# Kernel tuning notes

Hardware: AMD Instinct MI355X
Metric: run time of the kernel (lower is better)

## Reference

```python
import jax, jax.numpy as jnp
import numpy as np

D_MODEL = 1024
NUM_HEADS = 16
D_K = D_MODEL // NUM_HEADS
THETA = 10000.0
B, S = 2, 2048


def setup_inputs() -> dict:
    key = jax.random.key(0)
    k_x, k_q, k_k, k_v, k_o = jax.random.split(key, 5)
    std = np.sqrt(2.0 / (D_MODEL + D_MODEL))
    x = jax.random.normal(k_x, (B, S, D_MODEL), dtype=jnp.float32)
    # positions: per-row arange 0..S-1 (must stay < max_seq_len)
    token_positions = jnp.broadcast_to(jnp.arange(S, dtype=jnp.int32), (B, S))
    mk = lambda k: (jax.random.normal(k, (D_MODEL, D_MODEL), dtype=jnp.float32) * std)
    return {
        'x': x,
        'token_positions': token_positions,
        'Wq': mk(k_q), 'Wk': mk(k_k), 'Wv': mk(k_v), 'Wo': mk(k_o),
    }


def _rope(x, pos):
    # x: [B, H, S, D_K], pos: [B, S] int
    inv_freq = 1.0 / (THETA ** (jnp.arange(0, D_K, 2, dtype=jnp.float32) / D_K))  # [D_K/2]
    angles = pos.astype(jnp.float32)[..., None] * inv_freq  # [B, S, D_K/2]
    cos = jnp.cos(angles)[:, None, :, :]  # [B, 1, S, D_K/2]
    sin = jnp.sin(angles)[:, None, :, :]
    x_even = x[..., 0::2]
    x_odd = x[..., 1::2]
    out_even = x_even * cos - x_odd * sin
    out_odd = x_even * sin + x_odd * cos
    # interleave back: [..., D_K/2, 2] -> [..., D_K]
    return jnp.stack([out_even, out_odd], axis=-1).reshape(x.shape)


def reference(x, token_positions, Wq, Wk, Wv, Wo):
    b, s, d = x.shape
    h, dk = NUM_HEADS, D_K
    # projections: weight is [d_out, d_in], y = x W^T
    q = jnp.einsum('bsd,ed->bse', x, Wq).reshape(b, s, h, dk).transpose(0, 2, 1, 3)
    k = jnp.einsum('bsd,ed->bse', x, Wk).reshape(b, s, h, dk).transpose(0, 2, 1, 3)
    v = jnp.einsum('bsd,ed->bse', x, Wv).reshape(b, s, h, dk).transpose(0, 2, 1, 3)
    q = _rope(q, token_positions)
    k = _rope(k, token_positions)
    scores = jnp.einsum('bhqd,bhkd->bhqk', q, k) / jnp.sqrt(jnp.float32(dk))
    causal = jnp.tril(jnp.ones((s, s), dtype=bool))
    scores = jnp.where(causal, scores, -jnp.inf)
    weights = jax.nn.softmax(scores, axis=-1)
    attn = jnp.einsum('bhqk,bhkd->bhqd', weights, v)  # [B,H,S,D_K]
    concat = attn.transpose(0, 2, 1, 3).reshape(b, s, d)
    return jnp.einsum('bsd,ed->bse', concat, Wo)
```

## Files before the change

### kernel.cpp

```cpp
#include <hip/hip_runtime.h>
#include <hip/hip_bf16.h>

#define BB 2
#define SS 2048
#define DD 1024
#define HH 16
#define DKK 64
#define MM (BB * SS)
#define PER ((size_t)MM * DD)

typedef __bf16 v8bf __attribute__((ext_vector_type(8)));
typedef float  v4f  __attribute__((ext_vector_type(4)));

__device__ __forceinline__ float bf2f(unsigned int u16) {
    union { unsigned int i; float f; } x;
    x.i = u16 << 16;
    return x.f;
}
__device__ __forceinline__ unsigned int pack2(float a, float b) {
    union { __hip_bfloat16 h; unsigned short u; } x, y;
    x.h = __float2bfloat16(a); y.h = __float2bfloat16(b);
    return (unsigned int)x.u | ((unsigned int)y.u << 16);
}
__device__ __forceinline__ unsigned short f2bfu(float v) {
    union { __hip_bfloat16 h; unsigned short u; } x;
    x.h = __float2bfloat16(v);
    return x.u;
}
template<bool BF>
__device__ __forceinline__ void ld4(const void* p, size_t i, float* f) {
    if (BF) {
        const uint2 u = *(const uint2*)((const unsigned short*)p + i);
        f[0] = bf2f(u.x & 0xffffu); f[1] = bf2f(u.x >> 16);
        f[2] = bf2f(u.y & 0xffffu); f[3] = bf2f(u.y >> 16);
    } else {
        const float4 v = *(const float4*)((const float*)p + i);
        f[0] = v.x; f[1] = v.y; f[2] = v.z; f[3] = v.w;
    }
}
template<bool BF>
__device__ __forceinline__ void st1(void* p, size_t i, float v) {
    if (BF) ((__hip_bfloat16*)p)[i] = __float2bfloat16(v);
    else    ((float*)p)[i] = v;
}
template<bool BF>
__device__ __forceinline__ uint4 ld8bf(const void* p, size_t i) {
    if (BF) return *(const uint4*)((const unsigned short*)p + i);
    float f[8];
    ld4<false>(p, i, f);
    ld4<false>(p, i + 4, f + 4);
    uint4 u;
    u.x = pack2(f[0], f[1]); u.y = pack2(f[2], f[3]);
    u.z = pack2(f[4], f[5]); u.w = pack2(f[6], f[7]);
    return u;
}

typedef const __attribute__((address_space(1))) void* gas_p;
typedef __attribute__((address_space(3))) void* las_p;
__device__ __forceinline__ void gld16(const void* g, void* l) {
    __builtin_amdgcn_global_load_lds(
        (gas_p)(unsigned long long)g,
        (las_p)(unsigned int)(unsigned long long)l,
        16, 0, 0);
}

__device__ __forceinline__ bool sniff_bf(const void* x) {
    const unsigned int w = ((const unsigned int*)x)[threadIdx.x & 63];
    const int e = (w >> 7) & 0xFF;
    return __popcll(__ballot(e >= 100 && e <= 140)) >= 32;
}

__global__ __launch_bounds__(256) void precast(
    const void* __restrict__ X,  const void* __restrict__ Wq,
    const void* __restrict__ Wk, const void* __restrict__ Wv,
    const void* __restrict__ Wo, unsigned short* __restrict__ out,
    float* __restrict__ tab)
{
    const int bid = blockIdx.x;
    const int tid = threadIdx.x;

    if (bid >= 4096) {
        const int idx = (bid - 4096) * 256 + tid;
        const int s = idx >> 5;
        const int f = idx & 31;
        const float invf = __expf((float)f * -0.2878231366f);
        const float ang = (float)s * invf;
        float sn, cs;
        __sincosf(ang, &sn, &cs);
        ((float2*)tab)[idx] = make_float2(cs, sn);
        return;
    }

    const void* src;
    size_t off;
    unsigned short* dst;
    if (bid < 2048) {
        src = X;
        off = (size_t)bid * 2048;
        dst = out + off;
    } else {
        const int w  = (bid - 2048) >> 9;
        const size_t lo = (size_t)((bid - 2048) & 511) * 2048;
        src = (w == 0) ? Wq : (w == 1) ? Wk : (w == 2) ? Wv : Wo;
        off = lo;
        dst = out + PER + (size_t)w * (DD * DD) + lo;
    }
    const bool bf = sniff_bf(src);
    const size_t i = off + (size_t)tid * 8;
    if (bf) {
        *(uint4*)(dst + tid * 8) = *(const uint4*)((const unsigned short*)src + i);
    } else {
        float f[8];
        ld4<false>(src, i, f);
        ld4<false>(src, i + 4, f + 4);
        uint4 u;
        u.x = pack2(f[0], f[1]); u.y = pack2(f[2], f[3]);
        u.z = pack2(f[4], f[5]); u.w = pack2(f[6], f[7]);
        *(uint4*)(dst + tid * 8) = u;
    }
}

template<bool BF, bool TAB>
__device__ __forceinline__ void qkv_body128(
    const void* __restrict__ X,
    const void* __restrict__ Wq, const void* __restrict__ Wk, const void* __restrict__ Wv,
    const int* __restrict__ pos, const float* __restrict__ tab,
    __hip_bfloat16* __restrict__ Qb, __hip_bfloat16* __restrict__ Kb,
    __hip_bfloat16* __restrict__ Vb,
    unsigned short* Sh)
{
    const int tid  = threadIdx.x;
    const int lane = tid & 63;
    const int wv   = tid >> 6;
    const int wr   = wv >> 1;
    const int wc   = wv & 1;
    const int ln   = lane & 15;
    const int qd   = lane >> 4;
    const int srow = lane >> 2;
    const int sc4  = lane & 3;

    const int m0  = blockIdx.x * 128;
    const int n0g = blockIdx.y * 128;
    const int z   = n0g >> 10;
    const int nw  = n0g & (DD - 1);
    const void* W = (z == 0) ? Wq : (z == 1) ? Wk : Wv;

    unsigned short* A0 = Sh;
    unsigned short* A1 = Sh + 4096;
    unsigned short* B0 = Sh + 8192;
    unsigned short* B1 = Sh + 12288;

    auto stage = [&](int k0, unsigned short* Ad, unsigned short* Bd) {
#pragma unroll
        for (int g = 0; g < 2; ++g) {
            const int base = (wv * 2 + g) * 16;
            const int row  = base + srow;
            const int sc   = sc4 ^ ((row >> 1) & 3);
            const size_t ga = (size_t)(m0 + row) * DD + k0 + sc * 8;
            if (BF) gld16((const unsigned short*)X + ga, Ad + (size_t)base * 32);
            else    *(uint4*)(Ad + (size_t)row * 32 + sc4 * 8) = ld8bf<false>(X, ga);
            const size_t gb = (size_t)(nw + row) * DD + k0 + sc * 8;
            if (BF) gld16((const unsigned short*)W + gb, Bd + (size_t)base * 32);
            else    *(uint4*)(Bd + (size_t)row * 32 + sc4 * 8) = ld8bf<false>(W, gb);
        }
    };

    v4f acc[4][4];
#pragma unroll
    for (int i = 0; i < 4; ++i)
#pragma unroll
        for (int j = 0; j < 4; ++j) acc[i][j] = (v4f){0.f, 0.f, 0.f, 0.f};

    unsigned short *Ac = A0, *An = A1, *Bc = B0, *Bn = B1;
    stage(0, Ac, Bc);
    __syncthreads();

    const int rsw = (ln >> 1) & 3;

    for (int t = 0; t < 32; ++t) {
        if (t + 1 < 32) stage((t + 1) * 32, An, Bn);

        v8bf a[4], b[4];
#pragma unroll
        for (int mt = 0; mt < 4; ++mt)
            a[mt] = *(const v8bf*)&Ac[(size_t)(wr * 64 + mt * 16 + ln) * 32 +
                                      ((qd ^ rsw)) * 8];
#pragma unroll
        for (int nt = 0; nt < 4; ++nt)
            b[nt] = *(const v8bf*)&Bc[(size_t)(wc * 64 + nt * 16 + ln) * 32 +
                                      ((qd ^ rsw)) * 8];
#pragma unroll
        for (int mt = 0; mt < 4; ++mt)
#pragma unroll
            for (int nt = 0; nt < 4; ++nt)
                acc[mt][nt] = __builtin_amdgcn_mfma_f32_16x16x32_bf16(
                    a[mt], b[nt], acc[mt][nt], 0, 0, 0);

        __syncthreads();
        unsigned short* tp;
        tp = Ac; Ac = An; An = tp;
        tp = Bc; Bc = Bn; Bn = tp;
    }

    const int bb = m0 >> 11;
    if (z < 2) {
        __hip_bfloat16* Out = z ? Kb : Qb;
        const int head = (nw >> 6) + wc;
        float invf[4];
        if (!TAB) {
#pragma unroll
            for (int nt = 0; nt < 4; ++nt) {
                const int dk = nt * 16 + ln;
                invf[nt] = __expf((float)(dk >> 1) * -0.2878231366f);
            }
        }
#pragma unroll
        for (int mt = 0; mt < 4; ++mt) {
#pragma unroll
            for (int r = 0; r < 4; ++r) {
                const int m = m0 + wr * 64 + mt * 16 + qd * 4 + r;
                const int s = m & (SS - 1);
                const int pi = pos[m];
                const float p = (float)pi;
                const float2* trow = TAB ? ((const float2*)tab) + (size_t)pi * 32
                                         : nullptr;
#pragma unroll
                for (int nt = 0; nt < 4; ++nt) {
                    const int dk = nt * 16 + ln;
                    const float val = acc[mt][nt][r];
                    float sn, cs;
                    if (TAB) {
                        const float2 t2 = trow[nt * 8 + (ln >> 1)];
                        cs = t2.x; sn = t2.y;
                    } else {
                        const float ang = p * invf[nt];
                        __sincosf(ang, &sn, &cs);
                    }
                    const float prt = __shfl_xor(val, 1);
                    float res = ((dk & 1) == 0) ? (val * cs - prt * sn)
                                                : (prt * sn + val * cs);
                    if (z == 0) res *= 0.125f;
                    Out[((size_t)(bb * HH + head) * SS + s) * DKK + dk] =
                        __float2bfloat16(res);
                }
            }
        }
    } else {
        const int s0 = m0 & (SS - 1);
#pragma unroll
        for (int h2 = 0; h2 < 2; ++h2) {
            __syncthreads();
            if (wc == h2) {
#pragma unroll
                for (int nt = 0; nt < 4; ++nt)
#pragma unroll
                    for (int mt = 0; mt < 4; ++mt)
#pragma unroll
                        for (int r = 0; r < 4; ++r)
                            Sh[(size_t)(nt * 16 + ln) * 136 +
                               wr * 64 + mt * 16 + qd * 4 + r] =
                                f2bfu(acc[mt][nt][r]);
            }
            __syncthreads();
            const int head = (nw >> 6) + h2;
            const int row  = tid >> 2;
            const int c    = (tid & 3) * 32;
            unsigned short* dst = (unsigned short*)Vb +
                ((size_t)(bb * HH + head) * DKK + row) * SS + s0 + c;
            const unsigned short* Ts = Sh + (size_t)row * 136 + c;
#pragma unroll
            for (int j = 0; j < 4; ++j)
                *(uint4*)(dst + j * 8) = *(const uint4*)(Ts + j * 8);
        }
    }
}

__global__ __launch_bounds__(256) void qkv_gemm(
    const void* __restrict__ X,
    const void* __restrict__ Wq, const void* __restrict__ Wk, const void* __restrict__ Wv,
    const int* __restrict__ pos,
    __hip_bfloat16* __restrict__ Qb, __hip_bfloat16* __restrict__ Kb,
    __hip_bfloat16* __restrict__ Vb)
{
    __shared__ unsigned short Sh[16384];
    if (sniff_bf(X)) qkv_body128<true,  false>(X, Wq, Wk, Wv, pos, nullptr, Qb, Kb, Vb, Sh);
    else             qkv_body128<false, false>(X, Wq, Wk, Wv, pos, nullptr, Qb, Kb, Vb, Sh);
}

__global__ __launch_bounds__(256) void qkv_gemm_pc(
    const unsigned short* __restrict__ Xb,
    const unsigned short* __restrict__ Wqb, const unsigned short* __restrict__ Wkb,
    const unsigned short* __restrict__ Wvb,
    const int* __restrict__ pos, const float* __restrict__ tab,
    __hip_bfloat16* __restrict__ Qb, __hip_bfloat16* __restrict__ Kb,
    __hip_bfloat16* __restrict__ Vb)
{
    __shared__ unsigned short Sh[16384];
    qkv_body128<true, true>(Xb, Wqb, Wkb, Wvb, pos, tab, Qb, Kb, Vb, Sh);
}

__global__ __launch_bounds__(256) void attn_kernel(
    const __hip_bfloat16* __restrict__ Qb,
    const __hip_bfloat16* __restrict__ Kb,
    const __hip_bfloat16* __restrict__ Vtb,
    unsigned short* __restrict__ Ob, int olay)
{
    __shared__ unsigned short Ks[2][64 * 64];
    __shared__ unsigned short Vs[2][64 * 64];
    __shared__ unsigned short Ps[4][16 * 72];

    const int tid  = threadIdx.x;
    const int bh   = blockIdx.x & 31;
    const int qt   = 31 - (blockIdx.x >> 5);
    const int q0   = qt * 64;
    const int lane = tid & 63;
    const int wv   = tid >> 6;
    const int ln   = lane & 15;
    const int qd   = lane >> 4;
    const int r8   = lane >> 3;
    const int pc   = lane & 7;
    const int lchunk = pc ^ r8;

    const unsigned short* Qu = (const unsigned short*)Qb + (size_t)bh * SS * DKK;
    const unsigned short* Ku = (const unsigned short*)Kb + (size_t)bh * SS * DKK;
    const unsigned short* Vu = (const unsigned short*)Vtb + (size_t)bh * DKK * SS;

    const int qrow = q0 + wv * 16 + ln;
    const v8bf qf0 = *(const v8bf*)(Qu + (size_t)qrow * DKK + qd * 8);
    const v8bf qf1 = *(const v8bf*)(Qu + (size_t)qrow * DKK + 32 + qd * 8);

    auto stage = [&](int t, int b) {
        const int k0 = t * 64;
#pragma unroll
        for (int g = 0; g < 2; ++g) {
            const int row  = wv * 16 + g * 8 + r8;
            const int base = wv * 16 + g * 8;
            gld16(Ku + (size_t)(k0 + row) * DKK + lchunk * 8,
                  Ks[b] + (size_t)base * 64);
            gld16(Vu + (size_t)row * SS + k0 + lchunk * 8,
                  Vs[b] + (size_t)base * 64);
        }
    };

    v4f oacc[4];
#pragma unroll
    for (int n = 0; n < 4; ++n) oacc[n] = (v4f){0.f, 0.f, 0.f, 0.f};
    float lsum = 0.f;

    const int ntiles = qt + 1;
    const int qi = q0 + wv * 16 + ln;

    stage(0, 0);
    __syncthreads();

    for (int t = 0; t < ntiles; ++t) {
        const int cur = t & 1;
        if (t + 1 < ntiles) stage(t + 1, cur ^ 1);

        const unsigned short* Kc = Ks[cur];
        const unsigned short* Vc = Vs[cur];

        v4f s[4];
        __builtin_amdgcn_s_setprio(1);
#pragma unroll
        for (int g = 0; g < 4; ++g) {
            s[g] = (v4f){0.f, 0.f, 0.f, 0.f};
            const int krow = g * 16 + ln;
            const v8bf kf0 = *(const v8bf*)&Kc[(size_t)krow * 64 + ((qd ^ (ln & 7))) * 8];
            const v8bf kf1 = *(const v8bf*)&Kc[(size_t)krow * 64 + (((4 + qd) ^ (ln & 7))) * 8];
            s[g] = __builtin_amdgcn_mfma_f32_16x16x32_bf16(kf0, qf0, s[g], 0, 0, 0);
            s[g] = __builtin_amdgcn_mfma_f32_16x16x32_bf16(kf1, qf1, s[g], 0, 0, 0);
        }
        __builtin_amdgcn_s_setprio(0);

        const int k0 = t * 64;
        if (t == qt) {
#pragma unroll
            for (int g = 0; g < 4; ++g)
#pragma unroll
                for (int r = 0; r < 4; ++r) {
                    const int key = k0 + g * 16 + qd * 4 + r;
                    const float sv = (key <= qi) ? s[g][r] : -1e30f;
                    const float p = __expf(sv - 20.f);
                    s[g][r] = p;
                    lsum += p;
                }
        } else {
#pragma unroll
            for (int g = 0; g < 4; ++g)
#pragma unroll
                for (int r = 0; r < 4; ++r) {
                    const float p = __expf(s[g][r] - 20.f);
                    s[g][r] = p;
                    lsum += p;
                }
        }

        unsigned short* Pw = Ps[wv];
#pragma unroll
        for (int g = 0; g < 4; ++g) {
            uint2 w;
            w.x = pack2(s[g][0], s[g][1]);
            w.y = pack2(s[g][2], s[g][3]);
            *(uint2*)&Pw[(size_t)ln * 72 + g * 16 + qd * 4] = w;
        }

        const v8bf pf0 = *(const v8bf*)&Pw[(size_t)ln * 72 + qd * 8];
        const v8bf pf1 = *(const v8bf*)&Pw[(size_t)ln * 72 + 32 + qd * 8];
        __builtin_amdgcn_s_setprio(1);
#pragma unroll
        for (int n = 0; n < 4; ++n) {
            const int vrow = n * 16 + ln;
            const v8bf vf0 = *(const v8bf*)&Vc[(size_t)vrow * 64 + ((qd ^ (ln & 7))) * 8];
            const v8bf vf1 = *(const v8bf*)&Vc[(size_t)vrow * 64 + (((4 + qd) ^ (ln & 7))) * 8];
            oacc[n] = __builtin_amdgcn_mfma_f32_16x16x32_bf16(pf0, vf0, oacc[n], 0, 0, 0);
            oacc[n] = __builtin_amdgcn_mfma_f32_16x16x32_bf16(pf1, vf1, oacc[n], 0, 0, 0);
        }
        __builtin_amdgcn_s_setprio(0);

        __syncthreads();
    }

    lsum += __shfl_xor(lsum, 16);
    lsum += __shfl_xor(lsum, 32);

#pragma unroll
    for (int r = 0; r < 4; ++r) {
        const float inv = 1.f / __shfl(lsum, qd * 4 + r);
        const int row = q0 + wv * 16 + qd * 4 + r;
        unsigned short* op;
        if (olay) {
            op = Ob + ((size_t)((bh >> 4) * SS + row)) * DD + (bh & 15) * DKK;
        } else {
            op = Ob + ((size_t)bh * SS + row) * DKK;
        }
#pragma unroll
        for (int n = 0; n < 4; ++n)
            op[n * 16 + ln] = f2bfu(oacc[n][r] * inv);
    }
}

template<bool BFB, bool BFO, bool ACONT>
__device__ __forceinline__ void out_body128(
    const __hip_bfloat16* __restrict__ Ab, const void* __restrict__ Wo,
    void* __restrict__ Cb, float* __restrict__ Cf, int raw,
    unsigned short* Sh)
{
    const int tid  = threadIdx.x;
    const int lane = tid & 63;
    const int wv   = tid >> 6;
    const int wr   = wv >> 1;
    const int wc   = wv & 1;
    const int ln   = lane & 15;
    const int qd   = lane >> 4;
    const int r8   = lane >> 3;
    const int pc   = lane & 7;
    const int lchunk = pc ^ r8;

    const int m0 = blockIdx.x * 128, n0 = blockIdx.y * 128;
    const unsigned short* Au = (const unsigned short*)Ab;

    unsigned short* Abuf[2] = { Sh,               Sh + 2 * 8192 };
    unsigned short* Bbuf[2] = { Sh + 8192,        Sh + 3 * 8192 };

    auto stage = [&](int k0, unsigned short* Ad, unsigned short* Bd) {
#pragma unroll
        for (int g = 0; g < 4; ++g) {
            const int base = (wv * 4 + g) * 8;
            const int row  = base + r8;
            const int m = m0 + row;
            size_t ga;
            if (ACONT) ga = (size_t)m * DD + k0 + lchunk * 8;
            else       ga = ((size_t)((m >> 11) * HH + (k0 >> 6)) * SS + (m & (SS - 1))) * DKK
                            + lchunk * 8;
            gld16(Au + ga, Ad + (size_t)base * 64);
            const size_t gb = (size_t)(n0 + row) * DD + k0 + lchunk * 8;
            if (BFB) gld16((const unsigned short*)Wo + gb, Bd + (size_t)base * 64);
            else     *(uint4*)(Bd + (size_t)row * 64 + pc * 8) = ld8bf<false>(Wo, gb);
        }
    };

    v4f acc[4][4];
#pragma unroll
    for (int i = 0; i < 4; ++i)
#pragma unroll
        for (int j = 0; j < 4; ++j) acc[i][j] = (v4f){0.f, 0.f, 0.f, 0.f};

    stage(0, Abuf[0], Bbuf[0]);
    __syncthreads();

    for (int kk = 0; kk < 16; ++kk) {
        const int cur = kk & 1;
        if (kk + 1 < 16) stage((kk + 1) * 64, Abuf[cur ^ 1], Bbuf[cur ^ 1]);

        const unsigned short* As = Abuf[cur];
        const unsigned short* Bs = Bbuf[cur];
#pragma unroll
        for (int h = 0; h < 2; ++h) {
            v8bf a[4], b[4];
#pragma unroll
            for (int mt = 0; mt < 4; ++mt)
                a[mt] = *(const v8bf*)&As[(size_t)(wr * 64 + mt * 16 + ln) * 64 +
                                          (((h * 4 + qd) ^ (ln & 7))) * 8];
#pragma unroll
            for (int nt = 0; nt < 4; ++nt)
                b[nt] = *(const v8bf*)&Bs[(size_t)(wc * 64 + nt * 16 + ln) * 64 +
                                          (((h * 4 + qd) ^ (ln & 7))) * 8];
#pragma unroll
            for (int mt = 0; mt < 4; ++mt)
#pragma unroll
                for (int nt = 0; nt < 4; ++nt)
                    acc[mt][nt] = __builtin_amdgcn_mfma_f32_16x16x32_bf16(
                        a[mt], b[nt], acc[mt][nt], 0, 0, 0);
        }
        __syncthreads();
    }

#pragma unroll
    for (int mt = 0; mt < 4; ++mt) {
#pragma unroll
        for (int r = 0; r < 4; ++r) {
            const int m = m0 + wr * 64 + mt * 16 + qd * 4 + r;
#pragma unroll
            for (int nt = 0; nt < 4; ++nt) {
                const int e = n0 + wc * 64 + nt * 16 + ln;
                const size_t idx = (size_t)m * DD + e;
                const float v = acc[mt][nt][r];
                if (raw) Cf[idx] = v;
                else     st1<BFO>(Cb, idx, v);
            }
        }
    }
}

__global__ __launch_bounds__(256) void out_gemm(
    const __hip_bfloat16* __restrict__ Ab, const void* __restrict__ Wo,
    void* __restrict__ Cb, float* __restrict__ Cf, int raw,
    const void* __restrict__ xs)
{
    __shared__ unsigned short Sh[4 * 8192];
    if (sniff_bf(xs)) out_body128<true,  true,  false>(Ab, Wo, Cb, Cf, raw, Sh);
    else              out_body128<false, false, false>(Ab, Wo, Cb, Cf, raw, Sh);
}

__global__ __launch_bounds__(256) void out_gemm_pc(
    const __hip_bfloat16* __restrict__ Ab, const unsigned short* __restrict__ Wob,
    void* __restrict__ Cb, const void* __restrict__ xs)
{
    __shared__ unsigned short Sh[4 * 8192];
    if (sniff_bf(xs)) out_body128<true, true,  true>(Ab, Wob, Cb, nullptr, 0, Sh);
    else              out_body128<true, false, true>(Ab, Wob, Cb, nullptr, 0, Sh);
}

__global__ __launch_bounds__(256) void copy_cast(
    const float* __restrict__ src, void* __restrict__ dst, const void* __restrict__ xs)
{
    const bool bf = sniff_bf(xs);
    const size_t i = (size_t)blockIdx.x * 256 + threadIdx.x;
    const float v = src[i];
    if (bf) ((__hip_bfloat16*)dst)[i] = __float2bfloat16(v);
    else    ((float*)dst)[i] = v;
}

extern "C" void kernel_launch(void* const* d_in, const int* in_sizes, int n_in,
                              void* d_out, int out_size, void* d_ws, size_t ws_size,
                              hipStream_t stream) {
    (void)in_sizes; (void)n_in; (void)out_size;

    const void* x   = d_in[0];
    const int*  pos = (const int*)d_in[1];
    const void* Wq  = d_in[2];
    const void* Wk  = d_in[3];
    const void* Wv  = d_in[4];
    const void* Wo  = d_in[5];

    char* ws = (char*)d_ws;
    const size_t bpb   = PER * 2;
    const size_t castb = (PER + 4 * (size_t)DD * DD) * 2;
    const size_t tabb  = (size_t)SS * 32 * 2 * sizeof(float);
    const size_t need_full = 3 * bpb + castb + tabb + 64;

    if (ws_size >= need_full) {
        __hip_bfloat16* Qb = (__hip_bfloat16*)ws;
        __hip_bfloat16* Kb = Qb + PER;
        __hip_bfloat16* Vb = Kb + PER;
        unsigned short* cast = (unsigned short*)(ws + 3 * bpb);
        unsigned short* Xb  = cast;
        unsigned short* Wqb = cast + PER;
        unsigned short* Wkb = Wqb + (size_t)DD * DD;
        unsigned short* Wvb = Wkb + (size_t)DD * DD;
        unsigned short* Wob = Wvb + (size_t)DD * DD;
        float* tab = (float*)(cast + PER + 4 * (size_t)DD * DD);
        unsigned short* Obuf = Xb;

        precast<<<dim3(4352), 256, 0, stream>>>(x, Wq, Wk, Wv, Wo, cast, tab);

        dim3 g1(MM / 128, (3 * DD) / 128);
        qkv_gemm_pc<<<g1, 256, 0, stream>>>(Xb, Wqb, Wkb, Wvb, pos, tab, Qb, Kb, Vb);

        dim3 g2(32 * 32);
        attn_kernel<<<g2, 256, 0, stream>>>(Qb, Kb, Vb, Obuf, 1);

        dim3 g3(MM / 128, DD / 128);
        out_gemm_pc<<<g3, 256, 0, stream>>>((const __hip_bfloat16*)Obuf, Wob, d_out, x);
    } else if (ws_size >= 3 * bpb + 64) {
        __hip_bfloat16* Qb = (__hip_bfloat16*)ws;
        __hip_bfloat16* Kb = Qb + PER;
        __hip_bfloat16* Vb = Kb + PER;

        dim3 g1(MM / 128, (3 * DD) / 128);
        qkv_gemm<<<g1, 256, 0, stream>>>(x, Wq, Wk, Wv, pos, Qb, Kb, Vb);

        dim3 g2(32 * 32);
        attn_kernel<<<g2, 256, 0, stream>>>(Qb, Kb, Vb, (unsigned short*)Qb, 0);

        dim3 g3(MM / 128, DD / 128);
        out_gemm<<<g3, 256, 0, stream>>>(Qb, Wo, d_out, nullptr, 0, x);
    } else {
        __hip_bfloat16* Qb = (__hip_bfloat16*)d_out;
        __hip_bfloat16* Kb = (__hip_bfloat16*)ws;
        __hip_bfloat16* Vb = Kb + PER;
        float* Cf = (float*)ws;

        dim3 g1(MM / 128, (3 * DD) / 128);
        qkv_gemm<<<g1, 256, 0, stream>>>(x, Wq, Wk, Wv, pos, Qb, Kb, Vb);

        dim3 g2(32 * 32);
        attn_kernel<<<g2, 256, 0, stream>>>(Qb, Kb, Vb, (unsigned short*)Qb, 0);

        dim3 g3(MM / 128, DD / 128);
        out_gemm<<<g3, 256, 0, stream>>>(Qb, Wo, nullptr, Cf, 1, x);

        copy_cast<<<PER / 256, 256, 0, stream>>>(Cf, d_out, x);
    }
}
```

Measured before the change: 182.9 us.

## Widen QKV GEMM k-tile to 64 and pipeline loads with partial vmcnt waits

```diff
diff --git a/kernel.cpp b/kernel.cpp
--- a/kernel.cpp
+++ b/kernel.cpp
@@ -136,8 +136,9 @@
     const int wc   = wv & 1;
     const int ln   = lane & 15;
     const int qd   = lane >> 4;
-    const int srow = lane >> 2;
-    const int sc4  = lane & 3;
+    const int r8   = lane >> 3;
+    const int pc   = lane & 7;
+    const int lchunk = pc ^ r8;
 
     const int m0  = blockIdx.x * 128;
     const int n0g = blockIdx.y * 128;
@@ -145,23 +146,20 @@
     const int nw  = n0g & (DD - 1);
     const void* W = (z == 0) ? Wq : (z == 1) ? Wk : Wv;
 
-    unsigned short* A0 = Sh;
-    unsigned short* A1 = Sh + 4096;
-    unsigned short* B0 = Sh + 8192;
-    unsigned short* B1 = Sh + 12288;
+    unsigned short *Ac = Sh,         *An = Sh + 8192;
+    unsigned short *Bc = Sh + 16384, *Bn = Sh + 24576;
 
     auto stage = [&](int k0, unsigned short* Ad, unsigned short* Bd) {
 #pragma unroll
-        for (int g = 0; g < 2; ++g) {
-            const int base = (wv * 2 + g) * 16;
-            const int row  = base + srow;
-            const int sc   = sc4 ^ ((row >> 1) & 3);
-            const size_t ga = (size_t)(m0 + row) * DD + k0 + sc * 8;
-            if (BF) gld16((const unsigned short*)X + ga, Ad + (size_t)base * 32);
-            else    *(uint4*)(Ad + (size_t)row * 32 + sc4 * 8) = ld8bf<false>(X, ga);
-            const size_t gb = (size_t)(nw + row) * DD + k0 + sc * 8;
-            if (BF) gld16((const unsigned short*)W + gb, Bd + (size_t)base * 32);
-            else    *(uint4*)(Bd + (size_t)row * 32 + sc4 * 8) = ld8bf<false>(W, gb);
+        for (int g = 0; g < 4; ++g) {
+            const int base = (wv * 4 + g) * 8;
+            const int row  = base + r8;
+            const size_t ga = (size_t)(m0 + row) * DD + k0 + lchunk * 8;
+            if (BF) gld16((const unsigned short*)X + ga, Ad + (size_t)base * 64);
+            else    *(uint4*)(Ad + (size_t)row * 64 + pc * 8) = ld8bf<false>(X, ga);
+            const size_t gb = (size_t)(nw + row) * DD + k0 + lchunk * 8;
+            if (BF) gld16((const unsigned short*)W + gb, Bd + (size_t)base * 64);
+            else    *(uint4*)(Bd + (size_t)row * 64 + pc * 8) = ld8bf<false>(W, gb);
         }
     };
 
@@ -171,32 +169,49 @@
 #pragma unroll
         for (int j = 0; j < 4; ++j) acc[i][j] = (v4f){0.f, 0.f, 0.f, 0.f};
 
-    unsigned short *Ac = A0, *An = A1, *Bc = B0, *Bn = B1;
     stage(0, Ac, Bc);
-    __syncthreads();
-
-    const int rsw = (ln >> 1) & 3;
-
-    for (int t = 0; t < 32; ++t) {
-        if (t + 1 < 32) stage((t + 1) * 32, An, Bn);
-
-        v8bf a[4], b[4];
-#pragma unroll
-        for (int mt = 0; mt < 4; ++mt)
-            a[mt] = *(const v8bf*)&Ac[(size_t)(wr * 64 + mt * 16 + ln) * 32 +
-                                      ((qd ^ rsw)) * 8];
-#pragma unroll
-        for (int nt = 0; nt < 4; ++nt)
-            b[nt] = *(const v8bf*)&Bc[(size_t)(wc * 64 + nt * 16 + ln) * 32 +
-                                      ((qd ^ rsw)) * 8];
-#pragma unroll
-        for (int mt = 0; mt < 4; ++mt)
+
+    for (int t = 0; t < 16; ++t) {
+        const bool pf = (t + 1 < 16);
+        if (pf) stage((t + 1) * 64, An, Bn);
+
+        if (BF) {
+            if (pf) asm volatile("s_waitcnt vmcnt(8)" ::: "memory");
+            else    asm volatile("s_waitcnt vmcnt(0)" ::: "memory");
+            __builtin_amdgcn_s_barrier();
+            asm volatile("" ::: "memory");
+        } else {
+            __syncthreads();
+        }
+
+        __builtin_amdgcn_s_setprio(1);
+#pragma unroll
+        for (int h = 0; h < 2; ++h) {
+            v8bf a[4], b[4];
+#pragma unroll
+            for (int mt = 0; mt < 4; ++mt)
+                a[mt] = *(const v8bf*)&Ac[(size_t)(wr * 64 + mt * 16 + ln) * 64 +
+                                          (((h * 4 + qd) ^ (ln & 7))) * 8];
 #pragma unroll
             for (int nt = 0; nt < 4; ++nt)
-                acc[mt][nt] = __builtin_amdgcn_mfma_f32_16x16x32_bf16(
-                    a[mt], b[nt], acc[mt][nt], 0, 0, 0);
-
-        __syncthreads();
+                b[nt] = *(const v8bf*)&Bc[(size_t)(wc * 64 + nt * 16 + ln) * 64 +
+                                          (((h * 4 + qd) ^ (ln & 7))) * 8];
+#pragma unroll
+            for (int mt = 0; mt < 4; ++mt)
+#pragma unroll
+                for (int nt = 0; nt < 4; ++nt)
+                    acc[mt][nt] = __builtin_amdgcn_mfma_f32_16x16x32_bf16(
+                        a[mt], b[nt], acc[mt][nt], 0, 0, 0);
+        }
+        __builtin_amdgcn_s_setprio(0);
+
+        if (BF) {
+            asm volatile("" ::: "memory");
+            __builtin_amdgcn_s_barrier();
+        } else {
+            __syncthreads();
+        }
+
         unsigned short* tp;
         tp = Ac; Ac = An; An = tp;
         tp = Bc; Bc = Bn; Bn = tp;
@@ -282,7 +297,7 @@
     __hip_bfloat16* __restrict__ Qb, __hip_bfloat16* __restrict__ Kb,
     __hip_bfloat16* __restrict__ Vb)
 {
-    __shared__ unsigned short Sh[16384];
+    __shared__ unsigned short Sh[32768];
     if (sniff_bf(X)) qkv_body128<true,  false>(X, Wq, Wk, Wv, pos, nullptr, Qb, Kb, Vb, Sh);
     else             qkv_body128<false, false>(X, Wq, Wk, Wv, pos, nullptr, Qb, Kb, Vb, Sh);
 }
@@ -295,7 +310,7 @@
     __hip_bfloat16* __restrict__ Qb, __hip_bfloat16* __restrict__ Kb,
     __hip_bfloat16* __restrict__ Vb)
 {
-    __shared__ unsigned short Sh[16384];
+    __shared__ unsigned short Sh[32768];
     qkv_body128<true, true>(Xb, Wqb, Wkb, Wvb, pos, tab, Qb, Kb, Vb, Sh);
 }
 
@@ -460,8 +475,8 @@
     const int m0 = blockIdx.x * 128, n0 = blockIdx.y * 128;
     const unsigned short* Au = (const unsigned short*)Ab;
 
-    unsigned short* Abuf[2] = { Sh,               Sh + 2 * 8192 };
-    unsigned short* Bbuf[2] = { Sh + 8192,        Sh + 3 * 8192 };
+    unsigned short *Ac = Sh,         *An = Sh + 2 * 8192;
+    unsigned short *Bc = Sh + 8192,  *Bn = Sh + 3 * 8192;
 
     auto stage = [&](int k0, unsigned short* Ad, unsigned short* Bd) {
 #pragma unroll
@@ -486,25 +501,32 @@
 #pragma unroll
         for (int j = 0; j < 4; ++j) acc[i][j] = (v4f){0.f, 0.f, 0.f, 0.f};
 
-    stage(0, Abuf[0], Bbuf[0]);
-    __syncthreads();
+    stage(0, Ac, Bc);
 
     for (int kk = 0; kk < 16; ++kk) {
-        const int cur = kk & 1;
-        if (kk + 1 < 16) stage((kk + 1) * 64, Abuf[cur ^ 1], Bbuf[cur ^ 1]);
-
-        const unsigned short* As = Abuf[cur];
-        const unsigned short* Bs = Bbuf[cur];
+        const bool pf = (kk + 1 < 16);
+        if (pf) stage((kk + 1) * 64, An, Bn);
+
+        if (BFB) {
+            if (pf) asm volatile("s_waitcnt vmcnt(8)" ::: "memory");
+            else    asm volatile("s_waitcnt vmcnt(0)" ::: "memory");
+            __builtin_amdgcn_s_barrier();
+            asm volatile("" ::: "memory");
+        } else {
+            __syncthreads();
+        }
+
+        __builtin_amdgcn_s_setprio(1);
 #pragma unroll
         for (int h = 0; h < 2; ++h) {
             v8bf a[4], b[4];
 #pragma unroll
             for (int mt = 0; mt < 4; ++mt)
-                a[mt] = *(const v8bf*)&As[(size_t)(wr * 64 + mt * 16 + ln) * 64 +
+                a[mt] = *(const v8bf*)&Ac[(size_t)(wr * 64 + mt * 16 + ln) * 64 +
                                           (((h * 4 + qd) ^ (ln & 7))) * 8];
 #pragma unroll
             for (int nt = 0; nt < 4; ++nt)
-                b[nt] = *(const v8bf*)&Bs[(size_t)(wc * 64 + nt * 16 + ln) * 64 +
+                b[nt] = *(const v8bf*)&Bc[(size_t)(wc * 64 + nt * 16 + ln) * 64 +
                                           (((h * 4 + qd) ^ (ln & 7))) * 8];
 #pragma unroll
             for (int mt = 0; mt < 4; ++mt)
@@ -513,7 +535,18 @@
                     acc[mt][nt] = __builtin_amdgcn_mfma_f32_16x16x32_bf16(
                         a[mt], b[nt], acc[mt][nt], 0, 0, 0);
         }
-        __syncthreads();
+        __builtin_amdgcn_s_setprio(0);
+
+        if (BFB) {
+            asm volatile("" ::: "memory");
+            __builtin_amdgcn_s_barrier();
+        } else {
+            __syncthreads();
+        }
+
+        unsigned short* tp;
+        tp = Ac; Ac = An; An = tp;
+        tp = Bc; Bc = Bn; Bn = tp;
     }
 
 #pragma unroll
```

Result: faster. 166.6 us (median of 2 runs) (-8.9%).
